# Performance work log

Measured on AMD Instinct MI355X. Metric: run time of the kernel, lower is better.

## Reference

```python
import jax, jax.numpy as jnp
import numpy as np
import math

DIM = 1024
HEADS = 16
DH = DIM // HEADS
HIDDEN = 4 * DIM
B, N = 2, 1024
DT = 0.05


def _cplx(r, i):
    return jax.lax.complex(r, i)


def clin(x, Wr, Wi, br, bi):
    # complex linear: (xr + i xi)(Wr + i Wi)^T + (br + i bi)
    xr, xi = x.real, x.imag
    real = xr @ Wr.T - xi @ Wi.T + br
    imag = xr @ Wi.T + xi @ Wr.T + bi
    return _cplx(real, imag)


def setup_inputs() -> dict:
    key = jax.random.key(0)
    ks = jax.random.split(key, 32)
    s = 0.02
    d = {
        'x_real': jax.random.normal(ks[0], (B, N, DIM), jnp.float32),
        'x_imag': jax.random.normal(ks[1], (B, N, DIM), jnp.float32),
    }
    i = 2
    for name in ['q', 'k', 'v', 'o']:
        d[f'Wr_{name}'] = jax.random.normal(ks[i], (DIM, DIM), jnp.float32) * s; i += 1
        d[f'Wi_{name}'] = jax.random.normal(ks[i], (DIM, DIM), jnp.float32) * s; i += 1
        d[f'br_{name}'] = jnp.zeros((DIM,), jnp.float32)
        d[f'bi_{name}'] = jnp.zeros((DIM,), jnp.float32)
    d['Wr_f1'] = jax.random.normal(ks[i], (HIDDEN, DIM), jnp.float32) * s; i += 1
    d['Wi_f1'] = jax.random.normal(ks[i], (HIDDEN, DIM), jnp.float32) * s; i += 1
    d['br_f1'] = jnp.zeros((HIDDEN,), jnp.float32)
    d['bi_f1'] = jnp.zeros((HIDDEN,), jnp.float32)
    d['Wr_f2'] = jax.random.normal(ks[i], (DIM, HIDDEN), jnp.float32) * s; i += 1
    d['Wi_f2'] = jax.random.normal(ks[i], (DIM, HIDDEN), jnp.float32) * s; i += 1
    d['br_f2'] = jnp.zeros((DIM,), jnp.float32)
    d['bi_f2'] = jnp.zeros((DIM,), jnp.float32)
    H0 = jax.random.normal(ks[i], (DIM, DIM), jnp.float32) * s; i += 1
    d['H'] = (H0 + H0.T) / 2
    d['dt'] = jnp.float32(DT)
    return d


def _forward(x_real, x_imag,
             Wr_q, Wi_q, br_q, bi_q, Wr_k, Wi_k, br_k, bi_k,
             Wr_v, Wi_v, br_v, bi_v, Wr_o, Wi_o, br_o, bi_o,
             Wr_f1, Wi_f1, br_f1, bi_f1, Wr_f2, Wi_f2, br_f2, bi_f2,
             H, dt):
    x = _cplx(x_real, x_imag)  # [B,N,D] complex64
    scale = 1.0 / math.sqrt(DH)

    # --- Quantum Fourier attention ---
    def heads(t):
        return t.reshape(B, N, HEADS, DH).transpose(0, 2, 1, 3)  # [B,H,N,dh]
    Q = heads(clin(x, Wr_q, Wi_q, br_q, bi_q))
    K = heads(clin(x, Wr_k, Wi_k, br_k, bi_k))
    V = heads(clin(x, Wr_v, Wi_v, br_v, bi_v))
    Qf = jnp.fft.fft(Q, axis=2)
    Kf = jnp.fft.fft(K, axis=2)
    Vf = jnp.fft.fft(V, axis=2)
    scores = jnp.einsum('bhid,bhjd->bhij', Qf, jnp.conj(Kf)) * scale
    attn = jax.nn.softmax(scores.real, axis=-1).astype(jnp.complex64)
    out_f = jnp.einsum('bhij,bhjd->bhid', attn, Vf)
    out = jnp.fft.ifft(out_f, axis=2).transpose(0, 2, 1, 3).reshape(B, N, DIM)
    attn_out = clin(out, Wr_o, Wi_o, br_o, bi_o)
    x = x + attn_out

    # --- Quantum feed-forward (GELU on real & imag separately, exact erf) ---
    h = clin(x, Wr_f1, Wi_f1, br_f1, bi_f1)
    h = _cplx(jax.nn.gelu(h.real, approximate=False),
              jax.nn.gelu(h.imag, approximate=False))
    x = x + clin(h, Wr_f2, Wi_f2, br_f2, bi_f2)

    # --- Schrodinger unitary evolution: U = expm(-i H dt) ---
    A = _cplx(jnp.zeros_like(H), -(H * dt))  # complex64
    U = jax.scipy.linalg.expm(A)
    out = (x.reshape(B * N, DIM) @ U).reshape(B, N, DIM)
    return out


def reference(x_real, x_imag,
              Wr_q, Wi_q, br_q, bi_q, Wr_k, Wi_k, br_k, bi_k,
              Wr_v, Wi_v, br_v, bi_v, Wr_o, Wi_o, br_o, bi_o,
              Wr_f1, Wi_f1, br_f1, bi_f1, Wr_f2, Wi_f2, br_f2, bi_f2,
              H, dt):
    out = _forward(x_real, x_imag,
                   Wr_q, Wi_q, br_q, bi_q, Wr_k, Wi_k, br_k, bi_k,
                   Wr_v, Wi_v, br_v, bi_v, Wr_o, Wi_o, br_o, bi_o,
                   Wr_f1, Wi_f1, br_f1, bi_f1, Wr_f2, Wi_f2, br_f2, bi_f2,
                   H, dt)
    # return real/imag stacked for easy real-valued comparison: [2,B,N,D]
    return jnp.stack([out.real, out.imag], axis=0)
```

## Files before the change

### kernel.cpp

```cpp
#include <hip/hip_runtime.h>
#include <cstdint>
#include <cstddef>

typedef unsigned int u32;
typedef unsigned short u16;
typedef long long i64;

typedef __attribute__((ext_vector_type(8))) short short8;
typedef __attribute__((ext_vector_type(4))) float f32x4;
typedef __attribute__((ext_vector_type(4))) int i32x4;

__device__ __forceinline__ u16 f2bf(float f) {
  u32 u = __float_as_uint(f);
  u = (u + 0x7FFFu + ((u >> 16) & 1u)) >> 16;
  return (u16)u;
}
__device__ __forceinline__ float bf2f(u16 h) { return __uint_as_float(((u32)h) << 16); }

__device__ __forceinline__ short8 neg8(short8 v) {
  i32x4 u = __builtin_bit_cast(i32x4, v);
  u = u ^ (int)0x80008000u;
  return __builtin_bit_cast(short8, u);
}
__device__ __forceinline__ f32x4 mfma16(short8 a, short8 b, f32x4 c) {
  return __builtin_amdgcn_mfma_f32_16x16x32_bf16(a, b, c, 0, 0, 0);
}
__device__ __forceinline__ float gelu_f(float x) {
  return 0.5f * x * (1.0f + erff(x * 0.7071067811865475f));
}
__device__ __forceinline__ void gl16(const u16* g, u16* l) {
  __builtin_amdgcn_global_load_lds((const __attribute__((address_space(1))) void*)g,
                                   (__attribute__((address_space(3))) void*)l, 16, 0, 0);
}
template <int N>
__device__ __forceinline__ void wait_barrier() {
  asm volatile("s_waitcnt vmcnt(%0)\n\ts_barrier" ::"i"(N) : "memory");
}

struct GemmP {
  const u16 *Arh, *Aih, *Arl, *Ail;
  const u16 *Brh, *Bih, *Brl, *Bil;
  const float *biasr, *biasi;
  const float *Resr, *Resi;
  float *Cr32, *Ci32;
  u16 *Crh, *Cih, *Crl, *Cil;
  i64 sA1, sA2, sB1, sB2, sC1, sC2;
  int ZH;
  int M, N, K, lda, ldb, ldc;
  float alpha;
  int beta, wb32, ctrans, bias_mode, bias_period, gelu, splitB;
  float bias_scale;
};

template <int CMODE, int SPLIT>
__global__ __launch_bounds__(256, 2) void cgemm_kernel(GemmP p) {
  __shared__ u16 smem[SPLIT ? 24576 : 36864];
  constexpr bool HAS_CI = (CMODE == 0 || CMODE == 2 || CMODE == 3);
  constexpr bool AI = (CMODE == 0 || CMODE == 3);
  constexpr bool BIc = (CMODE == 0 || CMODE == 2 || CMODE == 3);
  constexpr int LPS = 3 + (AI ? 2 : 0) + (BIc ? 1 : 0);

  const int tid = threadIdx.x, lane = tid & 63, wave = tid >> 6;
  const int lrow = lane & 15, quad = lane >> 4;
  const int m0 = blockIdx.y * 128, n0 = blockIdx.x * 64;
  const int z1 = blockIdx.z / p.ZH, z2 = blockIdx.z % p.ZH;
  const i64 zA = (i64)z1 * p.sA1 + (i64)z2 * p.sA2;
  const i64 zB = (i64)z1 * p.sB1 + (i64)z2 * p.sB2;
  const i64 zC = (i64)z1 * p.sC1 + (i64)z2 * p.sC2;
  const int l4 = lane >> 2;
  const int lc = SPLIT ? ((lane & 3) << 3) : ((((lane & 3) ^ ((lane >> 3) & 3))) << 3);
  const i64 aoff0 = zA + (i64)(m0 + 32 * wave + l4) * p.lda + lc;
  const i64 aoff1 = aoff0 + (i64)16 * p.lda;
  const i64 boff = zB + (i64)(n0 + 16 * wave + l4) * p.ldb + lc;
  const int lA0 = (32 * wave) * 32, lA1 = lA0 + 512;
  const int lB0 = (16 * wave) * 32;

  f32x4 accR[2][4], accI[2][4];
  const f32x4 z4 = {0.f, 0.f, 0.f, 0.f};
#pragma unroll
  for (int i = 0; i < 2; ++i)
#pragma unroll
    for (int j = 0; j < 4; ++j) { accR[i][j] = z4; accI[i][j] = z4; }

  const int ktn = p.K >> 5;

  if constexpr (SPLIT) {
    for (int kt = 0; kt < ktn; ++kt) {
      const i64 kc = (i64)(kt << 5);
      __syncthreads();
      gl16(p.Arh + aoff0 + kc, smem + lA0);
      gl16(p.Arh + aoff1 + kc, smem + lA1);
      gl16(p.Aih + aoff0 + kc, smem + 4096 + lA0);
      gl16(p.Aih + aoff1 + kc, smem + 4096 + lA1);
      gl16(p.Arl + aoff0 + kc, smem + 8192 + lA0);
      gl16(p.Arl + aoff1 + kc, smem + 8192 + lA1);
      gl16(p.Ail + aoff0 + kc, smem + 12288 + lA0);
      gl16(p.Ail + aoff1 + kc, smem + 12288 + lA1);
      gl16(p.Brh + boff + kc, smem + 16384 + lB0);
      gl16(p.Bih + boff + kc, smem + 18432 + lB0);
      if (p.splitB) {
        gl16(p.Brl + boff + kc, smem + 20480 + lB0);
        gl16(p.Bil + boff + kc, smem + 22528 + lB0);
      }
      __syncthreads();

      short8 bRh[4], bIh[4], bRl[4], bIl[4];
#pragma unroll
      for (int j = 0; j < 4; ++j) {
        const int off = (j * 16 + lrow) * 32 + quad * 8;
        bRh[j] = *(const short8*)&smem[16384 + off];
        bIh[j] = *(const short8*)&smem[18432 + off];
        if (p.splitB) {
          bRl[j] = *(const short8*)&smem[20480 + off];
          bIl[j] = *(const short8*)&smem[22528 + off];
        }
      }
#pragma unroll
      for (int i = 0; i < 2; ++i) {
        const int off = (wave * 32 + i * 16 + lrow) * 32 + quad * 8;
        short8 aRh = *(const short8*)&smem[off];
        short8 aIh = *(const short8*)&smem[4096 + off];
        short8 aRl = *(const short8*)&smem[8192 + off];
        short8 aIl = *(const short8*)&smem[12288 + off];
        if constexpr (CMODE == 0) {
          short8 nIh = neg8(aIh), nIl = neg8(aIl);
#pragma unroll
          for (int j = 0; j < 4; ++j) {
            accR[i][j] = mfma16(aRh, bRh[j], accR[i][j]);
            accR[i][j] = mfma16(nIh, bIh[j], accR[i][j]);
            accI[i][j] = mfma16(aRh, bIh[j], accI[i][j]);
            accI[i][j] = mfma16(aIh, bRh[j], accI[i][j]);
            accR[i][j] = mfma16(aRl, bRh[j], accR[i][j]);
            accR[i][j] = mfma16(nIl, bIh[j], accR[i][j]);
            accI[i][j] = mfma16(aRl, bIh[j], accI[i][j]);
            accI[i][j] = mfma16(aIl, bRh[j], accI[i][j]);
            if (p.splitB) {
              accR[i][j] = mfma16(aRh, bRl[j], accR[i][j]);
              accR[i][j] = mfma16(nIh, bIl[j], accR[i][j]);
              accI[i][j] = mfma16(aRh, bIl[j], accI[i][j]);
              accI[i][j] = mfma16(aIh, bRl[j], accI[i][j]);
            }
          }
        } else {
#pragma unroll
          for (int j = 0; j < 4; ++j) {
            accR[i][j] = mfma16(aRh, bRh[j], accR[i][j]);
            accR[i][j] = mfma16(aIh, bIh[j], accR[i][j]);
            accR[i][j] = mfma16(aRl, bRh[j], accR[i][j]);
            accR[i][j] = mfma16(aIl, bIh[j], accR[i][j]);
            accR[i][j] = mfma16(aRh, bRl[j], accR[i][j]);
            accR[i][j] = mfma16(aIh, bIl[j], accR[i][j]);
          }
        }
      }
    }
  } else {
    auto stage = [&](int buf, i64 kc) {
      u16* s = smem + buf * 12288;
      gl16(p.Arh + aoff0 + kc, s + lA0);
      gl16(p.Arh + aoff1 + kc, s + lA1);
      if constexpr (AI) {
        gl16(p.Aih + aoff0 + kc, s + 4096 + lA0);
        gl16(p.Aih + aoff1 + kc, s + 4096 + lA1);
      }
      gl16(p.Brh + boff + kc, s + 8192 + lB0);
      if constexpr (BIc) gl16(p.Bih + boff + kc, s + 10240 + lB0);
    };
    const int cxw = ((lrow >> 1) & 3) << 3;
    if (ktn > 0) stage(0, 0);
    if (ktn > 1) stage(1, 32);
    for (int kt = 0; kt < ktn; ++kt) {
      if (kt + 1 < ktn) wait_barrier<LPS>(); else wait_barrier<0>();
      if (kt + 2 < ktn) stage((kt + 2) % 3, (i64)((kt + 2) << 5));
      const u16* sb = smem + (kt % 3) * 12288;

      short8 bR[4], bI[4];
#pragma unroll
      for (int j = 0; j < 4; ++j) {
        const int off = (j * 16 + lrow) * 32 + (quad * 8 ^ cxw);
        bR[j] = *(const short8*)&sb[8192 + off];
        if constexpr (BIc) bI[j] = *(const short8*)&sb[10240 + off];
      }
#pragma unroll
      for (int i = 0; i < 2; ++i) {
        const int off = (wave * 32 + i * 16 + lrow) * 32 + (quad * 8 ^ cxw);
        short8 aR = *(const short8*)&sb[off];
        if constexpr (CMODE == 0) {
          short8 aI = *(const short8*)&sb[4096 + off];
          short8 nI = neg8(aI);
#pragma unroll
          for (int j = 0; j < 4; ++j) {
            accR[i][j] = mfma16(aR, bR[j], accR[i][j]);
            accR[i][j] = mfma16(nI, bI[j], accR[i][j]);
            accI[i][j] = mfma16(aR, bI[j], accI[i][j]);
            accI[i][j] = mfma16(aI, bR[j], accI[i][j]);
          }
        } else if constexpr (CMODE == 1) {
#pragma unroll
          for (int j = 0; j < 4; ++j) accR[i][j] = mfma16(aR, bR[j], accR[i][j]);
        } else if constexpr (CMODE == 2) {
#pragma unroll
          for (int j = 0; j < 4; ++j) {
            accR[i][j] = mfma16(aR, bR[j], accR[i][j]);
            accI[i][j] = mfma16(aR, bI[j], accI[i][j]);
          }
        } else {
          short8 aI = *(const short8*)&sb[4096 + off];
          short8 nI = neg8(aI);
#pragma unroll
          for (int j = 0; j < 4; ++j) {
            accR[i][j] = mfma16(aR, bR[j], accR[i][j]);
            accR[i][j] = mfma16(aI, bI[j], accR[i][j]);
            accI[i][j] = mfma16(aR, bI[j], accI[i][j]);
            accI[i][j] = mfma16(nI, bR[j], accI[i][j]);
          }
        }
      }
    }
  }

#pragma unroll
  for (int i = 0; i < 2; ++i) {
#pragma unroll
    for (int j = 0; j < 4; ++j) {
      const int gn = n0 + j * 16 + lrow;
#pragma unroll
      for (int r = 0; r < 4; ++r) {
        const int gm = m0 + wave * 32 + i * 16 + quad * 4 + r;
        const i64 idx = p.ctrans ? (zC + (i64)gn * p.ldc + gm) : (zC + (i64)gm * p.ldc + gn);
        float vr = accR[i][j][r] * p.alpha;
        float vi = 0.f;
        if (HAS_CI) vi = accI[i][j][r] * p.alpha;
        if (p.beta) {
          vr += p.Cr32[idx];
          if (HAS_CI && p.Ci32) vi += p.Ci32[idx];
        }
        if (p.bias_mode == 1) {
          vr += p.biasr[gn];
          if (HAS_CI) vi += p.biasi[gn];
        } else if (p.bias_mode == 2) {
          if ((gm % p.bias_period) == 0) {
            vr += p.biasr[gn] * p.bias_scale;
            if (HAS_CI) vi += p.biasi[gn] * p.bias_scale;
          }
        }
        if (p.Resr) vr += p.Resr[idx];
        if (HAS_CI && p.Resi) vi += p.Resi[idx];
        if (p.gelu) {
          vr = gelu_f(vr);
          if (HAS_CI) vi = gelu_f(vi);
        }
        if (p.wb32 && p.Cr32) p.Cr32[idx] = vr;
        if (p.wb32 && HAS_CI && p.Ci32) p.Ci32[idx] = vi;
        if (p.Crh) {
          const u16 hh = f2bf(vr);
          p.Crh[idx] = hh;
          if (p.Crl) p.Crl[idx] = f2bf(vr - bf2f(hh));
        }
        if (HAS_CI && p.Cih) {
          const u16 hh = f2bf(vi);
          p.Cih[idx] = hh;
          if (p.Cil) p.Cil[idx] = f2bf(vi - bf2f(hh));
        }
      }
    }
  }
}

struct CvtBatch {
  const float* src[12];
  u16* hi[12];
  u16* lo[12];
  i64 cum[13];
};
__global__ __launch_bounds__(256) void cvt_batch_kernel(CvtBatch b) {
  const i64 k = (i64)blockIdx.x * 1024 + (i64)threadIdx.x * 4;
  int s = 0;
  while (k >= b.cum[s + 1]) ++s;
  const i64 base = k - b.cum[s];
  float4 v = *(const float4*)(b.src[s] + base);
  u16* hp = b.hi[s];
  u16* lp = b.lo[s];
  ushort4 h, l;
  h.x = f2bf(v.x); l.x = f2bf(v.x - bf2f(h.x));
  h.y = f2bf(v.y); l.y = f2bf(v.y - bf2f(h.y));
  h.z = f2bf(v.z); l.z = f2bf(v.z - bf2f(h.z));
  h.w = f2bf(v.w); l.w = f2bf(v.w - bf2f(h.w));
  *(ushort4*)(hp + base) = h;
  if (lp) *(ushort4*)(lp + base) = l;
}

__global__ __launch_bounds__(256) void cvt_split_kernel(const float* in, u16* hi, u16* lo,
                                                        i64 n, const float* scale_ptr) {
  const i64 base = (i64)blockIdx.x * 1024 + (i64)threadIdx.x * 4;
  const float s = scale_ptr ? *scale_ptr : 1.0f;
#pragma unroll
  for (int e = 0; e < 4; ++e) {
    const i64 k = base + e;
    if (k < n) {
      const float v = in[k] * s;
      const u16 h = f2bf(v);
      hi[k] = h;
      if (lo) lo[k] = f2bf(v - bf2f(h));
    }
  }
}

__global__ __launch_bounds__(256) void trans_cvt_kernel(const float* in, u16* outh, u16* outl) {
  __shared__ float t[32][33];
  const int b = blockIdx.z;
  const int j0 = blockIdx.y * 32;
  const int d0 = blockIdx.x * 32;
  const int r = threadIdx.x >> 5, c = threadIdx.x & 31;
  const float* ip = in + (i64)b * 1048576;
#pragma unroll
  for (int it = 0; it < 4; ++it) t[r + it * 8][c] = ip[(i64)(j0 + r + it * 8) * 1024 + d0 + c];
  __syncthreads();
  u16* ohp = outh + (i64)b * 1048576;
  u16* olp = outl + (i64)b * 1048576;
#pragma unroll
  for (int it = 0; it < 4; ++it) {
    const float v = t[c][r + it * 8];
    const i64 o = (i64)(d0 + r + it * 8) * 1024 + j0 + c;
    const u16 h = f2bf(v);
    ohp[o] = h;
    olp[o] = f2bf(v - bf2f(h));
  }
}

__global__ __launch_bounds__(256) void gen_F_kernel(u16* Frh, u16* Frl, u16* Fih, u16* Fil) {
  const int idx = blockIdx.x * 256 + threadIdx.x;
  const int mm = idx >> 10, kk = idx & 1023;
  const int t = (mm * kk) & 1023;
  float sv, cv;
  sincosf((float)t * 6.135923151e-3f, &sv, &cv);
  const float fr = cv, fi = -sv;
  u16 h = f2bf(fr);
  Frh[idx] = h;
  Frl[idx] = f2bf(fr - bf2f(h));
  h = f2bf(fi);
  Fih[idx] = h;
  Fil[idx] = f2bf(fi - bf2f(h));
}

__global__ __launch_bounds__(256) void assemble_U_kernel(const float* X2m, const float* Hm,
                                                         const float* dtp, u16* Urh, u16* Uih) {
  const int idx = blockIdx.x * 256 + threadIdx.x;
  const int i = idx >> 10, j = idx & 1023;
  const float dt = *dtp;
  const float ur = ((i == j) ? 1.0f : 0.0f) - 0.5f * X2m[idx];
  const float ui = -dt * Hm[idx];
  Urh[idx] = f2bf(ur);
  Uih[idx] = f2bf(ui);
}

__global__ __launch_bounds__(256) void softmax_kernel(float* S) {
  float* row = S + (i64)blockIdx.x * 1024;
  const int t = threadIdx.x;
  float4 v = *(float4*)(row + t * 4);
  float m = fmaxf(fmaxf(v.x, v.y), fmaxf(v.z, v.w));
#pragma unroll
  for (int off = 32; off > 0; off >>= 1) m = fmaxf(m, __shfl_down(m, off));
  __shared__ float red[8];
  const int lane = t & 63, w = t >> 6;
  if (lane == 0) red[w] = m;
  __syncthreads();
  if (t == 0) red[4] = fmaxf(fmaxf(red[0], red[1]), fmaxf(red[2], red[3]));
  __syncthreads();
  m = red[4];
  v.x = expf(v.x - m);
  v.y = expf(v.y - m);
  v.z = expf(v.z - m);
  v.w = expf(v.w - m);
  float s = v.x + v.y + v.z + v.w;
#pragma unroll
  for (int off = 32; off > 0; off >>= 1) s += __shfl_down(s, off);
  if (lane == 0) red[w] = s;
  __syncthreads();
  if (t == 0) red[5] = red[0] + red[1] + red[2] + red[3];
  __syncthreads();
  const float inv = 1.0f / red[5];
  ushort4 o;
  o.x = f2bf(v.x * inv);
  o.y = f2bf(v.y * inv);
  o.z = f2bf(v.z * inv);
  o.w = f2bf(v.w * inv);
  *(ushort4*)((u16*)row + t * 4) = o;
}

static void run_gemm(hipStream_t s, int cmode, int split, const GemmP& p, int Z) {
  dim3 g((unsigned)(p.N >> 6), (unsigned)(p.M >> 7), (unsigned)Z);
  dim3 b(256, 1, 1);
  const int key = cmode * 2 + split;
  if (key == 0) hipLaunchKernelGGL(HIP_KERNEL_NAME(cgemm_kernel<0, 0>), g, b, 0, s, p);
  else if (key == 1) hipLaunchKernelGGL(HIP_KERNEL_NAME(cgemm_kernel<0, 1>), g, b, 0, s, p);
  else if (key == 2) hipLaunchKernelGGL(HIP_KERNEL_NAME(cgemm_kernel<1, 0>), g, b, 0, s, p);
  else if (key == 3) hipLaunchKernelGGL(HIP_KERNEL_NAME(cgemm_kernel<1, 1>), g, b, 0, s, p);
  else if (key == 4) hipLaunchKernelGGL(HIP_KERNEL_NAME(cgemm_kernel<2, 0>), g, b, 0, s, p);
  else hipLaunchKernelGGL(HIP_KERNEL_NAME(cgemm_kernel<3, 0>), g, b, 0, s, p);
}

extern "C" void kernel_launch(void* const* d_in, const int* in_sizes, int n_in, void* d_out,
                              int out_size, void* d_ws, size_t ws_size, hipStream_t stream) {
  (void)in_sizes; (void)n_in; (void)out_size; (void)ws_size;
  const float* x_real = (const float*)d_in[0];
  const float* x_imag = (const float*)d_in[1];
  const float* Wr_q = (const float*)d_in[2];
  const float* Wi_q = (const float*)d_in[3];
  const float* br_q = (const float*)d_in[4];
  const float* bi_q = (const float*)d_in[5];
  const float* Wr_k = (const float*)d_in[6];
  const float* Wi_k = (const float*)d_in[7];
  const float* br_k = (const float*)d_in[8];
  const float* bi_k = (const float*)d_in[9];
  const float* Wr_v = (const float*)d_in[10];
  const float* Wi_v = (const float*)d_in[11];
  const float* br_v = (const float*)d_in[12];
  const float* bi_v = (const float*)d_in[13];
  const float* Wr_o = (const float*)d_in[14];
  const float* Wi_o = (const float*)d_in[15];
  const float* br_o = (const float*)d_in[16];
  const float* bi_o = (const float*)d_in[17];
  const float* Wr_f1 = (const float*)d_in[18];
  const float* Wi_f1 = (const float*)d_in[19];
  const float* br_f1 = (const float*)d_in[20];
  const float* bi_f1 = (const float*)d_in[21];
  const float* Wr_f2 = (const float*)d_in[22];
  const float* Wi_f2 = (const float*)d_in[23];
  const float* br_f2 = (const float*)d_in[24];
  const float* bi_f2 = (const float*)d_in[25];
  const float* Hm = (const float*)d_in[26];
  const float* dtp = (const float*)d_in[27];

  const size_t MBy = 1ull << 20;
  char* W = (char*)d_ws;
  auto U16 = [&](size_t mb) { return (u16*)(W + mb * MBy); };
  auto F32p = [&](size_t mb) { return (float*)(W + mb * MBy); };

  float* scores = F32p(0);
  u16 *xT_rh = U16(0), *xT_ih = U16(4), *xT_rl = U16(8), *xT_il = U16(12);
  u16 *Wq_rh = U16(16), *Wq_ih = U16(18), *Wq_rl = U16(20), *Wq_il = U16(22);
  u16 *Wk_rh = U16(24), *Wk_ih = U16(26), *Wk_rl = U16(28), *Wk_il = U16(30);
  u16 *xf_rh = U16(32), *xf_ih = U16(36), *xf_rl = U16(40), *xf_il = U16(44);
  u16 *h_r = U16(64), *h_i = U16(80);
  u16 *x2_rh = U16(96), *x2_ih = U16(100), *x2_rl = U16(104), *x2_il = U16(108);
  u16* Xh = U16(112);
  float* X2m = F32p(114);
  u16 *Urh = U16(124), *Uih = U16(126);
  u16 *Wv_rh = U16(128), *Wv_ih = U16(130);
  u16 *Wo_rh = U16(132), *Wo_ih = U16(134);
  u16 *Wf1_rh = U16(136), *Wf1_ih = U16(144);
  u16 *Wf2_rh = U16(152), *Wf2_ih = U16(160);
  u16 *F_rh = U16(168), *F_ih = U16(170), *F_rl = U16(172), *F_il = U16(174);
  u16 *Qf_rh = U16(176), *Qf_ih = U16(180), *Qf_rl = U16(184), *Qf_il = U16(188);
  u16 *Kf_rh = U16(192), *Kf_ih = U16(196), *Kf_rl = U16(200), *Kf_il = U16(204);
  u16 *VfT_r = U16(208), *VfT_i = U16(212);
  u16 *ofT_r = U16(216), *ofT_i = U16(220);
  u16 *ot_r = U16(224), *ot_i = U16(228);
  float* x1_r = F32p(232);
  float* x1_i = F32p(240);
  u16 *x1h_r = U16(248), *x1h_i = U16(252);

  {
    CvtBatch b{};
    const float* srcs[12] = {Wr_q, Wi_q, Wr_k, Wi_k, Wr_v, Wi_v, Wr_o, Wi_o,
                             Wr_f1, Wi_f1, Wr_f2, Wi_f2};
    u16* his[12] = {Wq_rh, Wq_ih, Wk_rh, Wk_ih, Wv_rh, Wv_ih, Wo_rh, Wo_ih,
                    Wf1_rh, Wf1_ih, Wf2_rh, Wf2_ih};
    u16* los[12] = {Wq_rl, Wq_il, Wk_rl, Wk_il, nullptr, nullptr, nullptr, nullptr,
                    nullptr, nullptr, nullptr, nullptr};
    const i64 sizes[12] = {1048576, 1048576, 1048576, 1048576, 1048576, 1048576, 1048576,
                           1048576, 4194304, 4194304, 4194304, 4194304};
    i64 c = 0;
    for (int i = 0; i < 12; ++i) {
      b.src[i] = srcs[i]; b.hi[i] = his[i]; b.lo[i] = los[i];
      b.cum[i] = c; c += sizes[i];
    }
    b.cum[12] = c;
    hipLaunchKernelGGL(cvt_batch_kernel, dim3((unsigned)(c / 1024)), dim3(256), 0, stream, b);
  }
  hipLaunchKernelGGL(trans_cvt_kernel, dim3(32, 32, 2), dim3(256), 0, stream, x_real, xT_rh, xT_rl);
  hipLaunchKernelGGL(trans_cvt_kernel, dim3(32, 32, 2), dim3(256), 0, stream, x_imag, xT_ih, xT_il);
  hipLaunchKernelGGL(gen_F_kernel, dim3(4096), dim3(256), 0, stream, F_rh, F_rl, F_ih, F_il);

  GemmP p;
  auto clearp = [&]() {
    p = GemmP{};
    p.alpha = 1.0f;
    p.ZH = 1;
  };

  clearp();
  p.M = 1024; p.N = 1024; p.K = 1024; p.lda = 1024; p.ldb = 1024; p.ldc = 1024;
  p.sB1 = 1048576; p.sC1 = 1048576;
  p.Arh = F_rh; p.Aih = F_ih; p.Arl = F_rl; p.Ail = F_il;
  p.Brh = xT_rh; p.Bih = xT_ih; p.Brl = xT_rl; p.Bil = xT_il; p.splitB = 1;
  p.Crh = xf_rh; p.Cih = xf_ih; p.Crl = xf_rl; p.Cil = xf_il;
  run_gemm(stream, 0, 1, p, 2);

  auto proj = [&](const u16* Wrh, const u16* Wih, const u16* Wrl, const u16* Wil,
                  const float* br, const float* bi, u16* Orh, u16* Oih, u16* Orl, u16* Oil) {
    clearp();
    p.M = 2048; p.N = 1024; p.K = 1024; p.lda = 1024; p.ldb = 1024; p.ldc = 1024;
    p.Arh = xf_rh; p.Aih = xf_ih; p.Arl = xf_rl; p.Ail = xf_il;
    p.Brh = Wrh; p.Bih = Wih; p.Brl = Wrl; p.Bil = Wil; p.splitB = 1;
    p.bias_mode = 2; p.bias_period = 1024; p.bias_scale = 1024.0f;
    p.biasr = br; p.biasi = bi;
    p.Crh = Orh; p.Cih = Oih; p.Crl = Orl; p.Cil = Oil;
    run_gemm(stream, 0, 1, p, 1);
  };
  proj(Wq_rh, Wq_ih, Wq_rl, Wq_il, br_q, bi_q, Qf_rh, Qf_ih, Qf_rl, Qf_il);
  proj(Wk_rh, Wk_ih, Wk_rl, Wk_il, br_k, bi_k, Kf_rh, Kf_ih, Kf_rl, Kf_il);

  clearp();
  p.M = 1024; p.N = 1024; p.K = 1024; p.lda = 1024; p.ldb = 1024; p.ldc = 1024;
  p.sA1 = 1048576; p.sC1 = 1048576;
  p.Arh = xf_rh; p.Aih = xf_ih; p.Brh = Wv_rh; p.Bih = Wv_ih;
  p.bias_mode = 2; p.bias_period = 1024; p.bias_scale = 1024.0f;
  p.biasr = br_v; p.biasi = bi_v;
  p.ctrans = 1;
  p.Crh = VfT_r; p.Cih = VfT_i;
  run_gemm(stream, 0, 0, p, 2);

  clearp();
  p.M = 1024; p.N = 1024; p.K = 64; p.lda = 1024; p.ldb = 1024; p.ldc = 1024;
  p.ZH = 16;
  p.sA1 = 1048576; p.sA2 = 64; p.sB1 = 1048576; p.sB2 = 64;
  p.sC1 = 16ll * 1048576; p.sC2 = 1048576;
  p.alpha = 0.125f;
  p.Arh = Qf_rh; p.Aih = Qf_ih; p.Arl = Qf_rl; p.Ail = Qf_il;
  p.Brh = Kf_rh; p.Bih = Kf_ih; p.Brl = Kf_rl; p.Bil = Kf_il; p.splitB = 1;
  p.Cr32 = scores; p.wb32 = 1;
  run_gemm(stream, 1, 1, p, 32);

  hipLaunchKernelGGL(softmax_kernel, dim3(32768), dim3(256), 0, stream, scores);

  clearp();
  p.M = 1024; p.N = 64; p.K = 1024; p.lda = 2048; p.ldb = 1024; p.ldc = 1024;
  p.ZH = 16;
  p.sA1 = 16ll * 2097152; p.sA2 = 2097152;
  p.sB1 = 1048576; p.sB2 = 65536;
  p.sC1 = 1048576; p.sC2 = 65536;
  p.ctrans = 1;
  p.Arh = (const u16*)scores; p.Brh = VfT_r; p.Bih = VfT_i;
  p.Crh = ofT_r; p.Cih = ofT_i;
  run_gemm(stream, 2, 0, p, 32);

  clearp();
  p.M = 1024; p.N = 1024; p.K = 1024; p.lda = 1024; p.ldb = 1024; p.ldc = 1024;
  p.sB1 = 1048576; p.sC1 = 1048576;
  p.alpha = 1.0f / 1024.0f;
  p.Arh = F_rh; p.Aih = F_ih; p.Brh = ofT_r; p.Bih = ofT_i;
  p.Crh = ot_r; p.Cih = ot_i;
  run_gemm(stream, 3, 0, p, 2);

  clearp();
  p.M = 2048; p.N = 1024; p.K = 1024; p.lda = 1024; p.ldb = 1024; p.ldc = 1024;
  p.Arh = ot_r; p.Aih = ot_i; p.Brh = Wo_rh; p.Bih = Wo_ih;
  p.bias_mode = 1; p.biasr = br_o; p.biasi = bi_o;
  p.Resr = x_real; p.Resi = x_imag;
  p.Cr32 = x1_r; p.Ci32 = x1_i; p.wb32 = 1; p.Crh = x1h_r; p.Cih = x1h_i;
  run_gemm(stream, 0, 0, p, 1);

  clearp();
  p.M = 2048; p.N = 4096; p.K = 1024; p.lda = 1024; p.ldb = 1024; p.ldc = 4096;
  p.Arh = x1h_r; p.Aih = x1h_i; p.Brh = Wf1_rh; p.Bih = Wf1_ih;
  p.bias_mode = 1; p.biasr = br_f1; p.biasi = bi_f1;
  p.gelu = 1;
  p.Crh = h_r; p.Cih = h_i;
  run_gemm(stream, 0, 0, p, 1);

  clearp();
  p.M = 2048; p.N = 1024; p.K = 4096; p.lda = 4096; p.ldb = 4096; p.ldc = 1024;
  p.Arh = h_r; p.Aih = h_i; p.Brh = Wf2_rh; p.Bih = Wf2_ih;
  p.bias_mode = 1; p.biasr = br_f2; p.biasi = bi_f2;
  p.Resr = x1_r; p.Resi = x1_i;
  p.Crh = x2_rh; p.Cih = x2_ih; p.Crl = x2_rl; p.Cil = x2_il;
  run_gemm(stream, 0, 0, p, 1);

  hipLaunchKernelGGL(cvt_split_kernel, dim3(1024), dim3(256), 0, stream, Hm, Xh,
                     (u16*)nullptr, (i64)1048576, dtp);

  clearp();
  p.M = 1024; p.N = 1024; p.K = 1024; p.lda = 1024; p.ldb = 1024; p.ldc = 1024;
  p.Arh = Xh; p.Brh = Xh;
  p.Cr32 = X2m; p.wb32 = 1;
  run_gemm(stream, 1, 0, p, 1);
  hipLaunchKernelGGL(assemble_U_kernel, dim3(4096), dim3(256), 0, stream, X2m, Hm, dtp, Urh, Uih);

  float* out_r = (float*)d_out;
  float* out_i = out_r + 2097152;
  clearp();
  p.M = 2048; p.N = 1024; p.K = 1024; p.lda = 1024; p.ldb = 1024; p.ldc = 1024;
  p.Arh = x2_rh; p.Aih = x2_ih; p.Arl = x2_rl; p.Ail = x2_il;
  p.Brh = Urh; p.Bih = Uih; p.splitB = 0;
  p.Cr32 = out_r; p.Ci32 = out_i; p.wb32 = 1;
  run_gemm(stream, 0, 1, p, 1);
}
```

Baseline: 1.016 ms.

## Add triple-buffered async pipeline for split-precision complex GEMM path

```diff
diff --git a/kernel.cpp b/kernel.cpp
--- a/kernel.cpp
+++ b/kernel.cpp
@@ -52,9 +52,11 @@
   float bias_scale;
 };
 
-template <int CMODE, int SPLIT>
+template <int CMODE, int SPLIT, int DEEP>
 __global__ __launch_bounds__(256, 2) void cgemm_kernel(GemmP p) {
-  __shared__ u16 smem[SPLIT ? 24576 : 36864];
+  constexpr int BUFU = SPLIT ? 24576 : 12288;
+  constexpr int NBUF = DEEP ? 3 : 1;
+  __shared__ u16 smem[BUFU * NBUF];
   constexpr bool HAS_CI = (CMODE == 0 || CMODE == 2 || CMODE == 3);
   constexpr bool AI = (CMODE == 0 || CMODE == 3);
   constexpr bool BIc = (CMODE == 0 || CMODE == 2 || CMODE == 3);
@@ -68,12 +70,13 @@
   const i64 zB = (i64)z1 * p.sB1 + (i64)z2 * p.sB2;
   const i64 zC = (i64)z1 * p.sC1 + (i64)z2 * p.sC2;
   const int l4 = lane >> 2;
-  const int lc = SPLIT ? ((lane & 3) << 3) : ((((lane & 3) ^ ((lane >> 3) & 3))) << 3);
+  const int lc = DEEP ? ((((lane & 3) ^ ((lane >> 3) & 3))) << 3) : ((lane & 3) << 3);
   const i64 aoff0 = zA + (i64)(m0 + 32 * wave + l4) * p.lda + lc;
   const i64 aoff1 = aoff0 + (i64)16 * p.lda;
   const i64 boff = zB + (i64)(n0 + 16 * wave + l4) * p.ldb + lc;
   const int lA0 = (32 * wave) * 32, lA1 = lA0 + 512;
   const int lB0 = (16 * wave) * 32;
+  const int cxw = ((lrow >> 1) & 3) << 3;
 
   f32x4 accR[2][4], accI[2][4];
   const f32x4 z4 = {0.f, 0.f, 0.f, 0.f};
@@ -84,7 +87,7 @@
 
   const int ktn = p.K >> 5;
 
-  if constexpr (SPLIT) {
+  if constexpr (SPLIT && !DEEP) {
     for (int kt = 0; kt < ktn; ++kt) {
       const i64 kc = (i64)(kt << 5);
       __syncthreads();
@@ -154,6 +157,85 @@
         }
       }
     }
+  } else if constexpr (SPLIT && DEEP) {
+    auto stageS = [&](int buf, i64 kc) {
+      u16* s = smem + buf * 24576;
+      gl16(p.Arh + aoff0 + kc, s + lA0);
+      gl16(p.Arh + aoff1 + kc, s + lA1);
+      gl16(p.Aih + aoff0 + kc, s + 4096 + lA0);
+      gl16(p.Aih + aoff1 + kc, s + 4096 + lA1);
+      gl16(p.Arl + aoff0 + kc, s + 8192 + lA0);
+      gl16(p.Arl + aoff1 + kc, s + 8192 + lA1);
+      gl16(p.Ail + aoff0 + kc, s + 12288 + lA0);
+      gl16(p.Ail + aoff1 + kc, s + 12288 + lA1);
+      gl16(p.Brh + boff + kc, s + 16384 + lB0);
+      gl16(p.Bih + boff + kc, s + 18432 + lB0);
+      if (p.splitB) {
+        gl16(p.Brl + boff + kc, s + 20480 + lB0);
+        gl16(p.Bil + boff + kc, s + 22528 + lB0);
+      }
+    };
+    if (ktn > 0) stageS(0, 0);
+    if (ktn > 1) stageS(1, 32);
+    for (int kt = 0; kt < ktn; ++kt) {
+      if (kt + 1 < ktn) {
+        if (p.splitB) wait_barrier<12>(); else wait_barrier<10>();
+      } else {
+        wait_barrier<0>();
+      }
+      if (kt + 2 < ktn) stageS((kt + 2) % 3, (i64)((kt + 2) << 5));
+      const u16* sb = smem + (kt % 3) * 24576;
+
+      short8 bRh[4], bIh[4], bRl[4], bIl[4];
+#pragma unroll
+      for (int j = 0; j < 4; ++j) {
+        const int off = (j * 16 + lrow) * 32 + (quad * 8 ^ cxw);
+        bRh[j] = *(const short8*)&sb[16384 + off];
+        bIh[j] = *(const short8*)&sb[18432 + off];
+        if (p.splitB) {
+          bRl[j] = *(const short8*)&sb[20480 + off];
+          bIl[j] = *(const short8*)&sb[22528 + off];
+        }
+      }
+#pragma unroll
+      for (int i = 0; i < 2; ++i) {
+        const int off = (wave * 32 + i * 16 + lrow) * 32 + (quad * 8 ^ cxw);
+        short8 aRh = *(const short8*)&sb[off];
+        short8 aIh = *(const short8*)&sb[4096 + off];
+        short8 aRl = *(const short8*)&sb[8192 + off];
+        short8 aIl = *(const short8*)&sb[12288 + off];
+        if constexpr (CMODE == 0) {
+          short8 nIh = neg8(aIh), nIl = neg8(aIl);
+#pragma unroll
+          for (int j = 0; j < 4; ++j) {
+            accR[i][j] = mfma16(aRh, bRh[j], accR[i][j]);
+            accR[i][j] = mfma16(nIh, bIh[j], accR[i][j]);
+            accI[i][j] = mfma16(aRh, bIh[j], accI[i][j]);
+            accI[i][j] = mfma16(aIh, bRh[j], accI[i][j]);
+            accR[i][j] = mfma16(aRl, bRh[j], accR[i][j]);
+            accR[i][j] = mfma16(nIl, bIh[j], accR[i][j]);
+            accI[i][j] = mfma16(aRl, bIh[j], accI[i][j]);
+            accI[i][j] = mfma16(aIl, bRh[j], accI[i][j]);
+            if (p.splitB) {
+              accR[i][j] = mfma16(aRh, bRl[j], accR[i][j]);
+              accR[i][j] = mfma16(nIh, bIl[j], accR[i][j]);
+              accI[i][j] = mfma16(aRh, bIl[j], accI[i][j]);
+              accI[i][j] = mfma16(aIh, bRl[j], accI[i][j]);
+            }
+          }
+        } else {
+#pragma unroll
+          for (int j = 0; j < 4; ++j) {
+            accR[i][j] = mfma16(aRh, bRh[j], accR[i][j]);
+            accR[i][j] = mfma16(aIh, bIh[j], accR[i][j]);
+            accR[i][j] = mfma16(aRl, bRh[j], accR[i][j]);
+            accR[i][j] = mfma16(aIl, bIh[j], accR[i][j]);
+            accR[i][j] = mfma16(aRh, bRl[j], accR[i][j]);
+            accR[i][j] = mfma16(aIh, bIl[j], accR[i][j]);
+          }
+        }
+      }
+    }
   } else {
     auto stage = [&](int buf, i64 kc) {
       u16* s = smem + buf * 12288;
@@ -166,7 +248,6 @@
       gl16(p.Brh + boff + kc, s + 8192 + lB0);
       if constexpr (BIc) gl16(p.Bih + boff + kc, s + 10240 + lB0);
     };
-    const int cxw = ((lrow >> 1) & 3) << 3;
     if (ktn > 0) stage(0, 0);
     if (ktn > 1) stage(1, 32);
     for (int kt = 0; kt < ktn; ++kt) {
@@ -388,16 +469,18 @@
   *(ushort4*)((u16*)row + t * 4) = o;
 }
 
-static void run_gemm(hipStream_t s, int cmode, int split, const GemmP& p, int Z) {
+static void run_gemm(hipStream_t s, int cmode, int split, int deep, const GemmP& p, int Z) {
   dim3 g((unsigned)(p.N >> 6), (unsigned)(p.M >> 7), (unsigned)Z);
   dim3 b(256, 1, 1);
-  const int key = cmode * 2 + split;
-  if (key == 0) hipLaunchKernelGGL(HIP_KERNEL_NAME(cgemm_kernel<0, 0>), g, b, 0, s, p);
-  else if (key == 1) hipLaunchKernelGGL(HIP_KERNEL_NAME(cgemm_kernel<0, 1>), g, b, 0, s, p);
-  else if (key == 2) hipLaunchKernelGGL(HIP_KERNEL_NAME(cgemm_kernel<1, 0>), g, b, 0, s, p);
-  else if (key == 3) hipLaunchKernelGGL(HIP_KERNEL_NAME(cgemm_kernel<1, 1>), g, b, 0, s, p);
-  else if (key == 4) hipLaunchKernelGGL(HIP_KERNEL_NAME(cgemm_kernel<2, 0>), g, b, 0, s, p);
-  else hipLaunchKernelGGL(HIP_KERNEL_NAME(cgemm_kernel<3, 0>), g, b, 0, s, p);
+  if (split) {
+    if (deep) hipLaunchKernelGGL(HIP_KERNEL_NAME(cgemm_kernel<0, 1, 1>), g, b, 0, s, p);
+    else hipLaunchKernelGGL(HIP_KERNEL_NAME(cgemm_kernel<1, 1, 0>), g, b, 0, s, p);
+  } else {
+    if (cmode == 0) hipLaunchKernelGGL(HIP_KERNEL_NAME(cgemm_kernel<0, 0, 1>), g, b, 0, s, p);
+    else if (cmode == 1) hipLaunchKernelGGL(HIP_KERNEL_NAME(cgemm_kernel<1, 0, 1>), g, b, 0, s, p);
+    else if (cmode == 2) hipLaunchKernelGGL(HIP_KERNEL_NAME(cgemm_kernel<2, 0, 1>), g, b, 0, s, p);
+    else hipLaunchKernelGGL(HIP_KERNEL_NAME(cgemm_kernel<3, 0, 1>), g, b, 0, s, p);
+  }
 }
 
 extern "C" void kernel_launch(void* const* d_in, const int* in_sizes, int n_in, void* d_out,
@@ -496,7 +579,7 @@
   p.Arh = F_rh; p.Aih = F_ih; p.Arl = F_rl; p.Ail = F_il;
   p.Brh = xT_rh; p.Bih = xT_ih; p.Brl = xT_rl; p.Bil = xT_il; p.splitB = 1;
   p.Crh = xf_rh; p.Cih = xf_ih; p.Crl = xf_rl; p.Cil = xf_il;
-  run_gemm(stream, 0, 1, p, 2);
+  run_gemm(stream, 0, 1, 1, p, 2);
 
   auto proj = [&](const u16* Wrh, const u16* Wih, const u16* Wrl, const u16* Wil,
                   const float* br, const float* bi, u16* Orh, u16* Oih, u16* Orl, u16* Oil) {
@@ -507,7 +590,7 @@
     p.bias_mode = 2; p.bias_period = 1024; p.bias_scale = 1024.0f;
     p.biasr = br; p.biasi = bi;
     p.Crh = Orh; p.Cih = Oih; p.Crl = Orl; p.Cil = Oil;
-    run_gemm(stream, 0, 1, p, 1);
+    run_gemm(stream, 0, 1, 1, p, 1);
   };
   proj(Wq_rh, Wq_ih, Wq_rl, Wq_il, br_q, bi_q, Qf_rh, Qf_ih, Qf_rl, Qf_il);
   proj(Wk_rh, Wk_ih, Wk_rl, Wk_il, br_k, bi_k, Kf_rh, Kf_ih, Kf_rl, Kf_il);
@@ -520,7 +603,7 @@
   p.biasr = br_v; p.biasi = bi_v;
   p.ctrans = 1;
   p.Crh = VfT_r; p.Cih = VfT_i;
-  run_gemm(stream, 0, 0, p, 2);
+  run_gemm(stream, 0, 0, 1, p, 2);
 
   clearp();
   p.M = 1024; p.N = 1024; p.K = 64; p.lda = 1024; p.ldb = 1024; p.ldc = 1024;
@@ -531,7 +614,7 @@
   p.Arh = Qf_rh; p.Aih = Qf_ih; p.Arl = Qf_rl; p.Ail = Qf_il;
   p.Brh = Kf_rh; p.Bih = Kf_ih; p.Brl = Kf_rl; p.Bil = Kf_il; p.splitB = 1;
   p.Cr32 = scores; p.wb32 = 1;
-  run_gemm(stream, 1, 1, p, 32);
+  run_gemm(stream, 1, 1, 0, p, 32);
 
   hipLaunchKernelGGL(softmax_kernel, dim3(32768), dim3(256), 0, stream, scores);
 
@@ -544,7 +627,7 @@
   p.ctrans = 1;
   p.Arh = (const u16*)scores; p.Brh = VfT_r; p.Bih = VfT_i;
   p.Crh = ofT_r; p.Cih = ofT_i;
-  run_gemm(stream, 2, 0, p, 32);
+  run_gemm(stream, 2, 0, 1, p, 32);
 
   clearp();
   p.M = 1024; p.N = 1024; p.K = 1024; p.lda = 1024; p.ldb = 1024; p.ldc = 1024;
@@ -552,7 +635,7 @@
   p.alpha = 1.0f / 1024.0f;
   p.Arh = F_rh; p.Aih = F_ih; p.Brh = ofT_r; p.Bih = ofT_i;
   p.Crh = ot_r; p.Cih = ot_i;
-  run_gemm(stream, 3, 0, p, 2);
+  run_gemm(stream, 3, 0, 1, p, 2);
 
   clearp();
   p.M = 2048; p.N = 1024; p.K = 1024; p.lda = 1024; p.ldb = 1024; p.ldc = 1024;
@@ -560,7 +643,7 @@
   p.bias_mode = 1; p.biasr = br_o; p.biasi = bi_o;
   p.Resr = x_real; p.Resi = x_imag;
   p.Cr32 = x1_r; p.Ci32 = x1_i; p.wb32 = 1; p.Crh = x1h_r; p.Cih = x1h_i;
-  run_gemm(stream, 0, 0, p, 1);
+  run_gemm(stream, 0, 0, 1, p, 1);
 
   clearp();
   p.M = 2048; p.N = 4096; p.K = 1024; p.lda = 1024; p.ldb = 1024; p.ldc = 4096;
@@ -568,7 +651,7 @@
   p.bias_mode = 1; p.biasr = br_f1; p.biasi = bi_f1;
   p.gelu = 1;
   p.Crh = h_r; p.Cih = h_i;
-  run_gemm(stream, 0, 0, p, 1);
+  run_gemm(stream, 0, 0, 1, p, 1);
 
   clearp();
   p.M = 2048; p.N = 1024; p.K = 4096; p.lda = 4096; p.ldb = 4096; p.ldc = 1024;
@@ -576,7 +659,7 @@
   p.bias_mode = 1; p.biasr = br_f2; p.biasi = bi_f2;
   p.Resr = x1_r; p.Resi = x1_i;
   p.Crh = x2_rh; p.Cih = x2_ih; p.Crl = x2_rl; p.Cil = x2_il;
-  run_gemm(stream, 0, 0, p, 1);
+  run_gemm(stream, 0, 0, 1, p, 1);
 
   hipLaunchKernelGGL(cvt_split_kernel, dim3(1024), dim3(256), 0, stream, Hm, Xh,
                      (u16*)nullptr, (i64)1048576, dtp);
@@ -585,7 +668,7 @@
   p.M = 1024; p.N = 1024; p.K = 1024; p.lda = 1024; p.ldb = 1024; p.ldc = 1024;
   p.Arh = Xh; p.Brh = Xh;
   p.Cr32 = X2m; p.wb32 = 1;
-  run_gemm(stream, 1, 0, p, 1);
+  run_gemm(stream, 1, 0, 1, p, 1);
   hipLaunchKernelGGL(assemble_U_kernel, dim3(4096), dim3(256), 0, stream, X2m, Hm, dtp, Urh, Uih);
 
   float* out_r = (float*)d_out;
@@ -595,5 +678,5 @@
   p.Arh = x2_rh; p.Aih = x2_ih; p.Arl = x2_rl; p.Ail = x2_il;
   p.Brh = Urh; p.Bih = Uih; p.splitB = 0;
   p.Cr32 = out_r; p.Ci32 = out_i; p.wb32 = 1;
-  run_gemm(stream, 0, 1, p, 1);
-}
+  run_gemm(stream, 0, 1, 1, p, 1);
+}
```

Result: faster. 969.3 us (-4.6%).
